# Kernel tuning notes

Measured on AMD Instinct MI355X. Metric: run time of the kernel, lower is better.

Reference implementation:

```python
import jax, jax.numpy as jnp
import numpy as np

W_SIZE = 5      # temporal_window_size
N_SUBSETS = 3   # graph adjacency subsets
PAD = (W_SIZE - 1) // 2
BN_EPS = 1e-5


def setup_inputs() -> dict:
    key = jax.random.key(0)
    k1, k2, k3, k4 = jax.random.split(key, 4)
    B, Cin, T, V = 32, 96, 288, 25
    Cout = 96
    x = jax.random.normal(k1, (B, Cin, T, V), dtype=jnp.float32)
    A = jax.random.uniform(k2, (N_SUBSETS, V, V), dtype=jnp.float32)
    conv_w = jax.random.normal(k3, (N_SUBSETS * Cout, Cin), dtype=jnp.float32) * 0.05
    conv_b = jax.random.normal(k4, (N_SUBSETS * Cout,), dtype=jnp.float32) * 0.05
    gamma = jnp.ones((Cout,), dtype=jnp.float32)
    beta = jnp.zeros((Cout,), dtype=jnp.float32)
    return {"x": x, "A": A, "conv_w": conv_w, "conv_b": conv_b,
            "gamma": gamma, "beta": beta}


def reference(x, A, conv_w, conv_b, gamma, beta):
    # x: (B, Cin, T, V); A: (S, V, V); conv_w: (S*Cout, Cin)
    B, Cin, T, V = x.shape
    S = N_SUBSETS
    Cout = conv_w.shape[0] // S

    # 1x1 conv: (B, S*Cout, T, V)
    y = jnp.einsum('bitv,oi->botv', x, conv_w) + conv_b[None, :, None, None]
    y = y.reshape(B, S, Cout, T, V)

    # Graph aggregation fused over subsets. The torch code tiles A along the
    # window axis and einsums 'bscfn,snm->bcfm' over the unfolded tensor; that
    # is mathematically (1/W) * sum_k sum_s sum_n y[b,s,c,f+k-pad,n] A[s,n,m].
    # Aggregate spatially first (sum over s and n), then window-sum in time.
    z = jnp.einsum('bsctn,snm->bctm', y, A)  # (B, Cout, T, V)

    # Temporal window sum with zero padding (stride=1, dilation=1).
    zp = jnp.pad(z, ((0, 0), (0, 0), (PAD, PAD), (0, 0)))
    out = zp[:, :, 0:T, :]
    for k in range(1, W_SIZE):
        out = out + zp[:, :, k:k + T, :]
    out = out * (1.0 / W_SIZE)

    # BatchNorm2d (training-mode batch statistics over B, T, V per channel)
    mean = jnp.mean(out, axis=(0, 2, 3), keepdims=True)
    var = jnp.var(out, axis=(0, 2, 3), keepdims=True)
    out = (out - mean) * jax.lax.rsqrt(var + BN_EPS)
    out = out * gamma[None, :, None, None] + beta[None, :, None, None]

    return jax.nn.relu(out)
```

## Files before the change

kernel.cpp:

```cpp
#include <hip/hip_runtime.h>
#include <hip/hip_bf16.h>

#define BB 32
#define CIN 96
#define TT 288
#define VV 25
#define SS 3
#define COUT 96
#define WSZ 5
#define BN_EPS 1e-5f
#define TV (TT*VV)
#define KK 288
#define XCOLS 64

typedef __attribute__((ext_vector_type(8))) short bf16x8;
typedef __attribute__((ext_vector_type(4))) float f32x4;

__device__ __forceinline__ unsigned short f2bf(float f) {
    unsigned u = __float_as_uint(f);
    return (unsigned short)((u + 0x7fffu + ((u >> 16) & 1u)) >> 16);
}

__global__ __launch_bounds__(256) void prep(
    const float* __restrict__ conv_w, const float* __restrict__ A,
    const float* __restrict__ cb,
    __hip_bfloat16* __restrict__ Wflat,
    __hip_bfloat16* __restrict__ Bfr,
    float* __restrict__ zbias,
    float* __restrict__ stats)
{
    int id = blockIdx.x*256 + threadIdx.x;
    if (id < 27648) {
        int c = id / KK, k = id - c*KK;
        int s = k / CIN, i = k - s*CIN;
        Wflat[id] = __float2bfloat16(conv_w[(s*COUT + c)*CIN + i]);
    } else if (id < 27648 + 3072) {
        int e = id - 27648;
        int f = e >> 9, rem = e & 511;
        int l = rem >> 3, j = rem & 7;
        int s = f >> 1, nt = f & 1;
        int n = (l >> 4)*8 + j;
        int m = nt*16 + (l & 15);
        float v = (n < VV && m < VV) ? A[(s*VV + n)*VV + m] : 0.0f;
        Bfr[e] = __float2bfloat16(v);
    } else if (id < 27648 + 3072 + 2400) {
        int e = id - 27648 - 3072;
        int c = e / VV, m = e - c*VV;
        float v = 0.f;
        #pragma unroll
        for (int s = 0; s < SS; ++s) {
            float sa = 0.f;
            #pragma unroll
            for (int n = 0; n < VV; ++n) sa += A[(s*VV + n)*VV + m];
            v = fmaf(cb[s*COUT + c], sa, v);
        }
        zbias[e] = v;
    } else if (id < 27648 + 3072 + 2400 + 192) {
        stats[id - 27648 - 3072 - 2400] = 0.0f;
    }
}

__global__ __launch_bounds__(256) void fused(
    const float* __restrict__ x,
    const __hip_bfloat16* __restrict__ Wflat,
    const __hip_bfloat16* __restrict__ Bfr,
    const float* __restrict__ zbias,
    float* __restrict__ out)
{
    __shared__ __hip_bfloat16 XAt[XCOLS*KK];
    const int tid  = threadIdx.x;
    const int lane = tid & 63;
    const int wave = tid >> 6;
    const int quad = lane >> 4;
    const int lrow = lane & 15;
    const int tile = blockIdx.x;
    const int b    = blockIdx.y;
    const int t0   = tile*2;

    bf16x8 bf1[6];
    #pragma unroll
    for (int f = 0; f < 6; ++f)
        bf1[f] = *(const bf16x8*)(Bfr + (f*64 + lane)*8);

    #pragma unroll
    for (int mt3 = 0; mt3 < 3; ++mt3) {
        const int Mtile = wave*3 + mt3;
        const int arow = Mtile*16 + lrow;
        const int ai = arow >> 1, atl = arow & 1;
        const float* xrow = x + ((size_t)(b*CIN + ai)*TT + (t0 + atl))*VV;
        float xv[8];
        if (quad < 3) {
            #pragma unroll
            for (int j = 0; j < 8; ++j) xv[j] = xrow[quad*8 + j];
        } else {
            #pragma unroll
            for (int j = 0; j < 8; ++j) xv[j] = 0.f;
            xv[0] = xrow[24];
        }
        bf16x8 af;
        #pragma unroll
        for (int j = 0; j < 8; ++j) ((short*)&af)[j] = (short)f2bf(xv[j]);

        const int i0 = Mtile*8 + quad*2;
        #pragma unroll
        for (int s = 0; s < SS; ++s) {
            #pragma unroll
            for (int nt = 0; nt < 2; ++nt) {
                f32x4 d = {0.f, 0.f, 0.f, 0.f};
                d = __builtin_amdgcn_mfma_f32_16x16x32_bf16(af, bf1[s*2+nt], d, 0, 0, 0);
                const int m = nt*16 + lrow;
                if (m < VV) {
                    const int k0 = s*CIN + i0;
                    const int g  = k0 >> 3, o = k0 & 7;
                    #pragma unroll
                    for (int tl = 0; tl < 2; ++tl) {
                        const int col = tl*VV + m;
                        const int gs  = (g & ~3) | ((g & 3) ^ ((col >> 1) & 3));
                        unsigned int pv = (unsigned int)f2bf(d[tl])
                                        | ((unsigned int)f2bf(d[tl+2]) << 16);
                        ((unsigned int*)XAt)[(col*KK + gs*8 + o) >> 1] = pv;
                    }
                }
            }
        }
    }
    __syncthreads();

    const int mh = wave & 1, nh = wave >> 1;
    f32x4 acc[3][2] = {};
    for (int it = 0; it < 9; ++it) {
        const int k0 = it*32;
        bf16x8 bfrag[2];
        #pragma unroll
        for (int ct = 0; ct < 2; ++ct) {
            const int cl = (nh*2 + ct)*16 + lrow;
            const int g0 = it*4 + (quad ^ ((cl >> 1) & 3));
            bfrag[ct] = *(const bf16x8*)&XAt[cl*KK + g0*8];
        }
        #pragma unroll
        for (int mt = 0; mt < 3; ++mt) {
            const int c = (mh*3 + mt)*16 + lrow;
            bf16x8 afrag = *(const bf16x8*)(Wflat + c*KK + k0 + quad*8);
            #pragma unroll
            for (int ct = 0; ct < 2; ++ct)
                acc[mt][ct] = __builtin_amdgcn_mfma_f32_16x16x32_bf16(
                    afrag, bfrag[ct], acc[mt][ct], 0, 0, 0);
        }
    }

    #pragma unroll
    for (int ct = 0; ct < 2; ++ct) {
        const int cl = (nh*2 + ct)*16 + lrow;
        if (cl < 2*VV) {
            const int tl = (cl >= VV) ? 1 : 0;
            const int m  = cl - tl*VV;
            float* obase = out + ((size_t)b*COUT*TT + (t0 + tl))*VV + m;
            #pragma unroll
            for (int mt = 0; mt < 3; ++mt) {
                const int cbase = (mh*3 + mt)*16 + quad*4;
                #pragma unroll
                for (int r = 0; r < 4; ++r) {
                    const int c = cbase + r;
                    obase[(size_t)c*TV] = acc[mt][ct][r] + zbias[c*VV + m];
                }
            }
        }
    }
}

__global__ __launch_bounds__(256) void k2_stats(
    const float* __restrict__ zbuf, float* __restrict__ ssum, float* __restrict__ ssq)
{
    __shared__ float zs[TV];
    __shared__ float red[8];
    const int tid = threadIdx.x;
    const int b = blockIdx.x / COUT;
    const int c = blockIdx.x - b*COUT;
    const float4* slab4 = (const float4*)(zbuf + (size_t)(b*COUT + c) * TV);
    float4* zs4 = (float4*)zs;
    for (int e = tid; e < TV/4; e += 256) zs4[e] = slab4[e];
    __syncthreads();

    float ls = 0.f, ls2 = 0.f;
    for (int e = tid; e < TV; e += 256) {
        int t = e / VV;
        float acc = zs[e];
        if (t >= 1)    acc += zs[e - VV];
        if (t >= 2)    acc += zs[e - 2*VV];
        if (t <= TT-2) acc += zs[e + VV];
        if (t <= TT-3) acc += zs[e + 2*VV];
        acc *= (1.0f / WSZ);
        ls  += acc;
        ls2 += acc * acc;
    }
    #pragma unroll
    for (int off = 32; off > 0; off >>= 1) {
        ls  += __shfl_down(ls,  off, 64);
        ls2 += __shfl_down(ls2, off, 64);
    }
    int lane = tid & 63, wid = tid >> 6;
    if (lane == 0) { red[wid*2] = ls; red[wid*2+1] = ls2; }
    __syncthreads();
    if (tid == 0) {
        atomicAdd(&ssum[c], red[0] + red[2] + red[4] + red[6]);
        atomicAdd(&ssq[c],  red[1] + red[3] + red[5] + red[7]);
    }
}

__global__ void k3_finalize(const float* __restrict__ ssum, const float* __restrict__ ssq,
                            const float* __restrict__ gamma, const float* __restrict__ beta,
                            float* __restrict__ scale, float* __restrict__ bias)
{
    int c = threadIdx.x;
    if (c < COUT) {
        const float invN = 1.0f / (float)(BB * TV);
        float mean = ssum[c] * invN;
        float var  = ssq[c] * invN - mean * mean;
        float inv  = rsqrtf(var + BN_EPS);
        float sc   = gamma[c] * inv;
        scale[c] = sc;
        bias[c]  = beta[c] - mean * sc;
    }
}

__global__ __launch_bounds__(256) void k4_win_norm(
    float* __restrict__ buf, const float* __restrict__ scale, const float* __restrict__ bias)
{
    __shared__ float zs[TV];
    const int tid = threadIdx.x;
    const int b = blockIdx.x / COUT;
    const int c = blockIdx.x - b*COUT;
    float* slab = buf + (size_t)(b*COUT + c) * TV;
    float4* slab4 = (float4*)slab;
    float4* zs4 = (float4*)zs;
    for (int e = tid; e < TV/4; e += 256) zs4[e] = slab4[e];
    __syncthreads();

    const float sc = scale[c], bi = bias[c];
    for (int u = tid; u < TV/4; u += 256) {
        float4 o;
        #pragma unroll
        for (int jj = 0; jj < 4; ++jj) {
            int e = u*4 + jj;
            int t = e / VV;
            float acc = zs[e];
            if (t >= 1)    acc += zs[e - VV];
            if (t >= 2)    acc += zs[e - 2*VV];
            if (t <= TT-2) acc += zs[e + VV];
            if (t <= TT-3) acc += zs[e + 2*VV];
            float val = fmaxf(fmaf(acc * (1.0f / WSZ), sc, bi), 0.0f);
            ((float*)&o)[jj] = val;
        }
        slab4[u] = o;
    }
}

extern "C" void kernel_launch(void* const* d_in, const int* in_sizes, int n_in,
                              void* d_out, int out_size, void* d_ws, size_t ws_size,
                              hipStream_t stream) {
    const float* x      = (const float*)d_in[0];
    const float* A      = (const float*)d_in[1];
    const float* conv_w = (const float*)d_in[2];
    const float* conv_b = (const float*)d_in[3];
    const float* gamma  = (const float*)d_in[4];
    const float* beta   = (const float*)d_in[5];
    float* out = (float*)d_out;

    float* zbias = (float*)d_ws;
    float* ssum  = zbias + 2400;
    float* ssq   = ssum + COUT;
    float* scale = ssq  + COUT;
    float* bias  = scale + COUT;
    __hip_bfloat16* Wflat = (__hip_bfloat16*)(bias + COUT);
    __hip_bfloat16* Bfr   = Wflat + (size_t)COUT * KK;

    prep <<<dim3(131),        dim3(256), 0, stream>>>(conv_w, A, conv_b, Wflat, Bfr, zbias, ssum);
    fused<<<dim3(TT/2, BB),   dim3(256), 0, stream>>>(x, Wflat, Bfr, zbias, out);
    k2_stats<<<dim3(BB*COUT), dim3(256), 0, stream>>>(out, ssum, ssq);
    k3_finalize<<<dim3(1),    dim3(128), 0, stream>>>(ssum, ssq, gamma, beta, scale, bias);
    k4_win_norm<<<dim3(BB*COUT), dim3(256), 0, stream>>>(out, scale, bias);
}
```

Measured before the change: 304.8 us.

## Move temporal window sum onto input before conv, drop finalize kernel

Because the 1x1 conv and the graph aggregation are linear, the temporal 5-tap window sum is applied to x while it loads, and the 1/5 factor is folded into the weights. The bias term is scaled by the count of valid taps at each boundary. This lets the stats and normalize kernels become plain streaming passes with no LDS staging or stencil, and the finalize kernel is merged into the normalize kernel. The cost is five times as many x loads in the fused kernel, though these are mostly cache hits, and every normalize block recomputes the per-channel scale.

```diff
diff --git a/kernel.cpp b/kernel.cpp
--- a/kernel.cpp
+++ b/kernel.cpp
@@ -33,7 +33,7 @@
     if (id < 27648) {
         int c = id / KK, k = id - c*KK;
         int s = k / CIN, i = k - s*CIN;
-        Wflat[id] = __float2bfloat16(conv_w[(s*COUT + c)*CIN + i]);
+        Wflat[id] = __float2bfloat16(0.2f * conv_w[(s*COUT + c)*CIN + i]);
     } else if (id < 27648 + 3072) {
         int e = id - 27648;
         int f = e >> 9, rem = e & 511;
@@ -87,15 +87,23 @@
         const int Mtile = wave*3 + mt3;
         const int arow = Mtile*16 + lrow;
         const int ai = arow >> 1, atl = arow & 1;
-        const float* xrow = x + ((size_t)(b*CIN + ai)*TT + (t0 + atl))*VV;
+        const int t  = t0 + atl;
+        const float* xr = x + ((size_t)(b*CIN + ai)*TT + t)*VV;
         float xv[8];
+        #pragma unroll
+        for (int j = 0; j < 8; ++j) xv[j] = 0.f;
         if (quad < 3) {
             #pragma unroll
-            for (int j = 0; j < 8; ++j) xv[j] = xrow[quad*8 + j];
+            for (int dt = -2; dt <= 2; ++dt) {
+                if ((unsigned)(t + dt) < TT) {
+                    #pragma unroll
+                    for (int j = 0; j < 8; ++j) xv[j] += xr[dt*VV + quad*8 + j];
+                }
+            }
         } else {
             #pragma unroll
-            for (int j = 0; j < 8; ++j) xv[j] = 0.f;
-            xv[0] = xrow[24];
+            for (int dt = -2; dt <= 2; ++dt)
+                if ((unsigned)(t + dt) < TT) xv[0] += xr[dt*VV + 24];
         }
         bf16x8 af;
         #pragma unroll
@@ -154,14 +162,18 @@
         if (cl < 2*VV) {
             const int tl = (cl >= VV) ? 1 : 0;
             const int m  = cl - tl*VV;
-            float* obase = out + ((size_t)b*COUT*TT + (t0 + tl))*VV + m;
+            const int t  = t0 + tl;
+            const int lo = (t-2 < 0) ? 0 : t-2;
+            const int hi = (t+2 > TT-1) ? TT-1 : t+2;
+            const float zs = (float)(hi - lo + 1) * 0.2f;
+            float* obase = out + ((size_t)b*COUT*TT + t)*VV + m;
             #pragma unroll
             for (int mt = 0; mt < 3; ++mt) {
                 const int cbase = (mh*3 + mt)*16 + quad*4;
                 #pragma unroll
                 for (int r = 0; r < 4; ++r) {
                     const int c = cbase + r;
-                    obase[(size_t)c*TV] = acc[mt][ct][r] + zbias[c*VV + m];
+                    obase[(size_t)c*TV] = acc[mt][ct][r] + zbias[c*VV + m] * zs;
                 }
             }
         }
@@ -171,34 +183,26 @@
 __global__ __launch_bounds__(256) void k2_stats(
     const float* __restrict__ zbuf, float* __restrict__ ssum, float* __restrict__ ssq)
 {
-    __shared__ float zs[TV];
     __shared__ float red[8];
-    const int tid = threadIdx.x;
-    const int b = blockIdx.x / COUT;
-    const int c = blockIdx.x - b*COUT;
-    const float4* slab4 = (const float4*)(zbuf + (size_t)(b*COUT + c) * TV);
-    float4* zs4 = (float4*)zs;
-    for (int e = tid; e < TV/4; e += 256) zs4[e] = slab4[e];
-    __syncthreads();
-
+    const int tid  = threadIdx.x;
+    const int slab = blockIdx.x;
+    const int c    = slab % COUT;
+    const float4* s4 = (const float4*)(zbuf + (size_t)slab * TV);
     float ls = 0.f, ls2 = 0.f;
-    for (int e = tid; e < TV; e += 256) {
-        int t = e / VV;
-        float acc = zs[e];
-        if (t >= 1)    acc += zs[e - VV];
-        if (t >= 2)    acc += zs[e - 2*VV];
-        if (t <= TT-2) acc += zs[e + VV];
-        if (t <= TT-3) acc += zs[e + 2*VV];
-        acc *= (1.0f / WSZ);
-        ls  += acc;
-        ls2 += acc * acc;
+    for (int e = tid; e < TV/4; e += 256) {
+        float4 v = s4[e];
+        ls  += (v.x + v.y) + (v.z + v.w);
+        ls2 = fmaf(v.x, v.x, ls2);
+        ls2 = fmaf(v.y, v.y, ls2);
+        ls2 = fmaf(v.z, v.z, ls2);
+        ls2 = fmaf(v.w, v.w, ls2);
     }
     #pragma unroll
     for (int off = 32; off > 0; off >>= 1) {
         ls  += __shfl_down(ls,  off, 64);
         ls2 += __shfl_down(ls2, off, 64);
     }
-    int lane = tid & 63, wid = tid >> 6;
+    const int lane = tid & 63, wid = tid >> 6;
     if (lane == 0) { red[wid*2] = ls; red[wid*2+1] = ls2; }
     __syncthreads();
     if (tid == 0) {
@@ -207,51 +211,27 @@
     }
 }
 
-__global__ void k3_finalize(const float* __restrict__ ssum, const float* __restrict__ ssq,
-                            const float* __restrict__ gamma, const float* __restrict__ beta,
-                            float* __restrict__ scale, float* __restrict__ bias)
-{
-    int c = threadIdx.x;
-    if (c < COUT) {
-        const float invN = 1.0f / (float)(BB * TV);
-        float mean = ssum[c] * invN;
-        float var  = ssq[c] * invN - mean * mean;
-        float inv  = rsqrtf(var + BN_EPS);
-        float sc   = gamma[c] * inv;
-        scale[c] = sc;
-        bias[c]  = beta[c] - mean * sc;
-    }
-}
-
-__global__ __launch_bounds__(256) void k4_win_norm(
-    float* __restrict__ buf, const float* __restrict__ scale, const float* __restrict__ bias)
-{
-    __shared__ float zs[TV];
-    const int tid = threadIdx.x;
-    const int b = blockIdx.x / COUT;
-    const int c = blockIdx.x - b*COUT;
-    float* slab = buf + (size_t)(b*COUT + c) * TV;
-    float4* slab4 = (float4*)slab;
-    float4* zs4 = (float4*)zs;
-    for (int e = tid; e < TV/4; e += 256) zs4[e] = slab4[e];
-    __syncthreads();
-
-    const float sc = scale[c], bi = bias[c];
+__global__ __launch_bounds__(256) void k4_norm(
+    float* __restrict__ buf, const float* __restrict__ ssum, const float* __restrict__ ssq,
+    const float* __restrict__ gamma, const float* __restrict__ beta)
+{
+    const int tid  = threadIdx.x;
+    const int slab = blockIdx.x;
+    const int c    = slab % COUT;
+    const float invN = 1.0f / (float)(BB * TV);
+    const float mean = ssum[c] * invN;
+    const float var  = ssq[c] * invN - mean * mean;
+    const float inv  = rsqrtf(var + BN_EPS);
+    const float sc   = gamma[c] * inv;
+    const float bi   = beta[c] - mean * sc;
+    float4* p = (float4*)(buf + (size_t)slab * TV);
     for (int u = tid; u < TV/4; u += 256) {
-        float4 o;
-        #pragma unroll
-        for (int jj = 0; jj < 4; ++jj) {
-            int e = u*4 + jj;
-            int t = e / VV;
-            float acc = zs[e];
-            if (t >= 1)    acc += zs[e - VV];
-            if (t >= 2)    acc += zs[e - 2*VV];
-            if (t <= TT-2) acc += zs[e + VV];
-            if (t <= TT-3) acc += zs[e + 2*VV];
-            float val = fmaxf(fmaf(acc * (1.0f / WSZ), sc, bi), 0.0f);
-            ((float*)&o)[jj] = val;
-        }
-        slab4[u] = o;
+        float4 v = p[u];
+        v.x = fmaxf(fmaf(v.x, sc, bi), 0.0f);
+        v.y = fmaxf(fmaf(v.y, sc, bi), 0.0f);
+        v.z = fmaxf(fmaf(v.z, sc, bi), 0.0f);
+        v.w = fmaxf(fmaf(v.w, sc, bi), 0.0f);
+        p[u] = v;
     }
 }
 
@@ -269,14 +249,11 @@
     float* zbias = (float*)d_ws;
     float* ssum  = zbias + 2400;
     float* ssq   = ssum + COUT;
-    float* scale = ssq  + COUT;
-    float* bias  = scale + COUT;
-    __hip_bfloat16* Wflat = (__hip_bfloat16*)(bias + COUT);
+    __hip_bfloat16* Wflat = (__hip_bfloat16*)(ssq + COUT);
     __hip_bfloat16* Bfr   = Wflat + (size_t)COUT * KK;
 
-    prep <<<dim3(131),        dim3(256), 0, stream>>>(conv_w, A, conv_b, Wflat, Bfr, zbias, ssum);
-    fused<<<dim3(TT/2, BB),   dim3(256), 0, stream>>>(x, Wflat, Bfr, zbias, out);
-    k2_stats<<<dim3(BB*COUT), dim3(256), 0, stream>>>(out, ssum, ssq);
-    k3_finalize<<<dim3(1),    dim3(128), 0, stream>>>(ssum, ssq, gamma, beta, scale, bias);
-    k4_win_norm<<<dim3(BB*COUT), dim3(256), 0, stream>>>(out, scale, bias);
-}
+    prep    <<<dim3(131),        dim3(256), 0, stream>>>(conv_w, A, conv_b, Wflat, Bfr, zbias, ssum);
+    fused   <<<dim3(TT/2, BB),   dim3(256), 0, stream>>>(x, Wflat, Bfr, zbias, out);
+    k2_stats<<<dim3(BB*COUT),    dim3(256), 0, stream>>>(out, ssum, ssq);
+    k4_norm <<<dim3(BB*COUT),    dim3(256), 0, stream>>>(out, ssum, ssq, gamma, beta);
+}
```

After: 312.0 us. +2.4%, slower.
